# Optimization experiments

Hardware: AMD Instinct MI355X
Metric: run time of the kernel (lower is better)

The kernel has to match this reference:

```python
import jax, jax.numpy as jnp
import numpy as np

ORDER = 2


def _masked_row_mean(v, m, safe_cnt, has_any):
    # v already zeroed outside mask; per-row mean over masked entries
    s = jnp.sum(v, axis=1, keepdims=True) / safe_cnt
    return jnp.where(has_any, s, 0.0)


def high_order_residual(x, mask, order=ORDER):
    """Vectorized faithful version of high_order_residual (braq).
    nanmean over masked entries == masked sum / count; sign/scale/shift
    are only meaningful inside the mask, outputs outside the mask are 0.
    """
    m = mask.astype(x.dtype)                       # (oc, ic)
    cnt = jnp.sum(m, axis=1, keepdims=True)        # (oc, 1)
    safe_cnt = jnp.maximum(cnt, 1.0)
    has_any = cnt > 0
    xm = x * m
    sum_order = jnp.zeros_like(x)
    for _ in range(order):
        residual = (xm - sum_order) * m            # masked residual, 0 outside
        mean = _masked_row_mean(residual, m, safe_cnt, has_any)   # (oc,1)
        centered = (residual - mean) * m           # 0 outside mask
        scale = _masked_row_mean(jnp.abs(centered), m, safe_cnt, has_any)
        binary = jnp.sign(centered) * scale + mean
        sum_order = sum_order + binary * m
    return sum_order


def setup_inputs() -> dict:
    key = jax.random.key(0)
    k1, k2 = jax.random.split(key)
    x = jax.random.normal(k1, (11008, 4096), dtype=jnp.float32) * 0.02
    mask = jax.random.randint(k2, (11008, 4096), 0, 2).astype(jnp.bool_)
    return {"x": x, "mask": mask}


def reference(x, mask):
    return high_order_residual(x, mask, ORDER)
```

## Files before the change

kernel.cpp:

```cpp
#include <hip/hip_runtime.h>
#include <stdint.h>

#define IC      4096
#define BLK     256
#define RPB     4
#define CHUNKS  16
#define EPT     64

__global__ __launch_bounds__(BLK) void binarize_kernel(
    const float* __restrict__ x,
    const uint8_t* __restrict__ mask,
    float* __restrict__ out,
    int nrows)
{
    const int lane = threadIdx.x & 63;
    const int row  = blockIdx.x * RPB + (threadIdx.x >> 6);
    if (row >= nrows) return;

    const bool mask_is_i32 = !__any(((const uint32_t*)mask)[lane] > 1u);

    const float* xr   = x   + (size_t)row * IC;
    float*       orow = out + (size_t)row * IC;

    float xm[EPT];
    #pragma unroll
    for (int i = 0; i < CHUNKS; ++i) {
        float4 v = ((const float4*)xr)[lane + 64 * i];
        xm[4*i+0] = v.x; xm[4*i+1] = v.y; xm[4*i+2] = v.z; xm[4*i+3] = v.w;
    }

    uint32_t mw0 = 0, mw1 = 0;
    if (mask_is_i32) {
        const int4* mr = (const int4*)mask + (size_t)row * (IC / 4);
        #pragma unroll
        for (int i = 0; i < CHUNKS; ++i) {
            int4 m4 = mr[lane + 64 * i];
            uint32_t b = (uint32_t)(m4.x != 0)
                       | ((uint32_t)(m4.y != 0) << 1)
                       | ((uint32_t)(m4.z != 0) << 2)
                       | ((uint32_t)(m4.w != 0) << 3);
            if (i < 8) mw0 |= b << (4 * i);
            else       mw1 |= b << (4 * (i - 8));
        }
    } else {
        const uint32_t* mr = (const uint32_t*)(mask + (size_t)row * IC);
        #pragma unroll
        for (int i = 0; i < CHUNKS; ++i) {
            uint32_t w = mr[lane + 64 * i];
            uint32_t b = (uint32_t)((w & 0x000000ffu) != 0)
                       | ((uint32_t)((w & 0x0000ff00u) != 0) << 1)
                       | ((uint32_t)((w & 0x00ff0000u) != 0) << 2)
                       | ((uint32_t)((w & 0xff000000u) != 0) << 3);
            if (i < 8) mw0 |= b << (4 * i);
            else       mw1 |= b << (4 * (i - 8));
        }
    }

    #pragma unroll
    for (int j = 0; j < EPT; ++j) {
        const uint32_t bit = ((j < 32 ? mw0 : mw1) >> (j & 31)) & 1u;
        xm[j] = bit ? xm[j] : 0.f;
    }

    double sA0 = 0.0, sA1 = 0.0;
    #pragma unroll
    for (int j = 0; j < EPT; j += 2) {
        sA0 += (double)xm[j];
        sA1 += (double)xm[j + 1];
    }
    double s  = sA0 + sA1;
    float  cf = (float)(__popc(mw0) + __popc(mw1));
    #pragma unroll
    for (int off = 32; off; off >>= 1) {
        s  += __shfl_xor(s,  off);
        cf += __shfl_xor(cf, off);
    }

    const bool   has    = (cf > 0.f);
    const double c      = (double)cf;
    const double nmiss  = (double)(4096.f - cf);
    const double inv    = 1.0 / fmax(c, 1.0);
    const double mean1  = has ? s * inv : 0.0;
    const float  mean1f = (float)mean1;

    double saB0 = 0.0, saB1 = 0.0;
    float  dB0 = 0.f, dB1 = 0.f;
    #pragma unroll
    for (int j = 0; j < EPT; ++j) {
        const uint32_t bit = ((j < 32 ? mw0 : mw1) >> (j & 31)) & 1u;
        const float t   = xm[j] - mean1f;
        const float sg  = (t > 0.f) ? 1.f : ((t < 0.f) ? -1.f : 0.f);
        const float smv = bit ? sg : 0.f;
        if (j & 1) { dB1 += smv; saB1 += (double)fabsf(t); }
        else       { dB0 += smv; saB0 += (double)fabsf(t); }
    }
    double sa = saB0 + saB1;
    float  df = dB0 + dB1;
    #pragma unroll
    for (int off = 32; off; off >>= 1) {
        sa += __shfl_xor(sa, off);
        df += __shfl_xor(df, off);
    }
    sa -= nmiss * (double)fabsf(mean1f);

    const double scale1 = has ? sa * inv : 0.0;
    const double mean2  = has ? (s - scale1 * (double)df - mean1 * c) * inv : 0.0;
    const double mean12 = mean1 + mean2;

    double sb0 = 0.0, sb1 = 0.0;
    #pragma unroll
    for (int j = 0; j < EPT; ++j) {
        const uint32_t bit = ((j < 32 ? mw0 : mw1) >> (j & 31)) & 1u;
        const float t   = xm[j] - mean1f;
        const float sg  = (t > 0.f) ? 1.f : ((t < 0.f) ? -1.f : 0.f);
        const float smv = bit ? sg : 0.f;
        const double t2 = (double)xm[j] - fma((double)smv, scale1, mean12);
        if (j & 1) sb1 += fabs(t2); else sb0 += fabs(t2);
    }
    double sa2 = sb0 + sb1;
    #pragma unroll
    for (int off = 32; off; off >>= 1) sa2 += __shfl_xor(sa2, off);
    sa2 -= nmiss * fabs(mean12);
    const double scale2  = has ? sa2 * inv : 0.0;
    const float  scale2f = (float)scale2;

    #pragma unroll
    for (int i = 0; i < CHUNKS; ++i) {
        float r[4];
        #pragma unroll
        for (int k = 0; k < 4; ++k) {
            const int j = 4 * i + k;
            const uint32_t bit = ((j < 32 ? mw0 : mw1) >> (j & 31)) & 1u;
            const float t   = xm[j] - mean1f;
            const float sg  = (t > 0.f) ? 1.f : ((t < 0.f) ? -1.f : 0.f);
            const float smv = bit ? sg : 0.f;
            const double t2 = (double)xm[j] - fma((double)smv, scale1, mean12);
            const float t2f = (float)t2;
            const float b1f = xm[j] - t2f;
            const float sg2 = (t2f > 0.f) ? 1.f : ((t2f < 0.f) ? -1.f : 0.f);
            const float o   = fmaf(sg2, scale2f, b1f);
            r[k] = bit ? o : 0.f;
        }
        float4 o4; o4.x = r[0]; o4.y = r[1]; o4.z = r[2]; o4.w = r[3];
        ((float4*)orow)[lane + 64 * i] = o4;
    }
}

extern "C" void kernel_launch(void* const* d_in, const int* in_sizes, int n_in,
                              void* d_out, int out_size, void* d_ws, size_t ws_size,
                              hipStream_t stream) {
    const float*   x    = (const float*)d_in[0];
    const uint8_t* mask = (const uint8_t*)d_in[1];
    float*         out  = (float*)d_out;

    const int rows = in_sizes[0] / IC;
    const int grid = (rows + RPB - 1) / RPB;
    binarize_kernel<<<grid, BLK, 0, stream>>>(x, mask, out, rows);
}
```

Baseline: 418.1 us.

## Re-read row from global per pass instead of holding it in registers

The 64-element per-thread register array holding the masked row is removed. Each of the four passes now reloads the row from global memory (expected to hit in cache) and re-applies the mask bits. Launch bounds now request a minimum of 4 blocks per CU, which should allow more waves to be resident and better hide latency. The cost is three extra row reads per pass, served from L2 or the infinity cache, and a risk of becoming bandwidth-bound if those reads miss.

```diff
diff --git a/kernel.cpp b/kernel.cpp
--- a/kernel.cpp
+++ b/kernel.cpp
@@ -3,72 +3,60 @@
 
 #define IC      4096
 #define BLK     256
-#define RPB     4
+#define WPB     4
 #define CHUNKS  16
-#define EPT     64
 
-__global__ __launch_bounds__(BLK) void binarize_kernel(
+__global__ __launch_bounds__(BLK, 4) void binarize_kernel(
     const float* __restrict__ x,
     const uint8_t* __restrict__ mask,
     float* __restrict__ out,
     int nrows)
 {
     const int lane = threadIdx.x & 63;
-    const int row  = blockIdx.x * RPB + (threadIdx.x >> 6);
+    const int row  = blockIdx.x * WPB + (threadIdx.x >> 6);
     if (row >= nrows) return;
 
     const bool mask_is_i32 = !__any(((const uint32_t*)mask)[lane] > 1u);
 
-    const float* xr   = x   + (size_t)row * IC;
-    float*       orow = out + (size_t)row * IC;
-
-    float xm[EPT];
-    #pragma unroll
-    for (int i = 0; i < CHUNKS; ++i) {
-        float4 v = ((const float4*)xr)[lane + 64 * i];
-        xm[4*i+0] = v.x; xm[4*i+1] = v.y; xm[4*i+2] = v.z; xm[4*i+3] = v.w;
-    }
+    const float4* xr4 = (const float4*)(x + (size_t)row * IC);
+    float4*       or4 = (float4*)(out + (size_t)row * IC);
 
     uint32_t mw0 = 0, mw1 = 0;
+    double sacc[4] = {0.0, 0.0, 0.0, 0.0};
     if (mask_is_i32) {
         const int4* mr = (const int4*)mask + (size_t)row * (IC / 4);
         #pragma unroll
         for (int i = 0; i < CHUNKS; ++i) {
-            int4 m4 = mr[lane + 64 * i];
-            uint32_t b = (uint32_t)(m4.x != 0)
-                       | ((uint32_t)(m4.y != 0) << 1)
-                       | ((uint32_t)(m4.z != 0) << 2)
-                       | ((uint32_t)(m4.w != 0) << 3);
-            if (i < 8) mw0 |= b << (4 * i);
-            else       mw1 |= b << (4 * (i - 8));
+            const float4 v  = xr4[lane + 64 * i];
+            const int4   m4 = mr[lane + 64 * i];
+            const uint32_t b = (uint32_t)(m4.x != 0)
+                             | ((uint32_t)(m4.y != 0) << 1)
+                             | ((uint32_t)(m4.z != 0) << 2)
+                             | ((uint32_t)(m4.w != 0) << 3);
+            if (i < 8) mw0 |= b << (4 * i); else mw1 |= b << (4 * (i - 8));
+            sacc[0] += (double)((b & 1u) ? v.x : 0.f);
+            sacc[1] += (double)((b & 2u) ? v.y : 0.f);
+            sacc[2] += (double)((b & 4u) ? v.z : 0.f);
+            sacc[3] += (double)((b & 8u) ? v.w : 0.f);
         }
     } else {
         const uint32_t* mr = (const uint32_t*)(mask + (size_t)row * IC);
         #pragma unroll
         for (int i = 0; i < CHUNKS; ++i) {
-            uint32_t w = mr[lane + 64 * i];
-            uint32_t b = (uint32_t)((w & 0x000000ffu) != 0)
-                       | ((uint32_t)((w & 0x0000ff00u) != 0) << 1)
-                       | ((uint32_t)((w & 0x00ff0000u) != 0) << 2)
-                       | ((uint32_t)((w & 0xff000000u) != 0) << 3);
-            if (i < 8) mw0 |= b << (4 * i);
-            else       mw1 |= b << (4 * (i - 8));
+            const float4   v = xr4[lane + 64 * i];
+            const uint32_t w = mr[lane + 64 * i];
+            const uint32_t b = (uint32_t)((w & 0x000000ffu) != 0)
+                             | ((uint32_t)((w & 0x0000ff00u) != 0) << 1)
+                             | ((uint32_t)((w & 0x00ff0000u) != 0) << 2)
+                             | ((uint32_t)((w & 0xff000000u) != 0) << 3);
+            if (i < 8) mw0 |= b << (4 * i); else mw1 |= b << (4 * (i - 8));
+            sacc[0] += (double)((b & 1u) ? v.x : 0.f);
+            sacc[1] += (double)((b & 2u) ? v.y : 0.f);
+            sacc[2] += (double)((b & 4u) ? v.z : 0.f);
+            sacc[3] += (double)((b & 8u) ? v.w : 0.f);
         }
     }
-
-    #pragma unroll
-    for (int j = 0; j < EPT; ++j) {
-        const uint32_t bit = ((j < 32 ? mw0 : mw1) >> (j & 31)) & 1u;
-        xm[j] = bit ? xm[j] : 0.f;
-    }
-
-    double sA0 = 0.0, sA1 = 0.0;
-    #pragma unroll
-    for (int j = 0; j < EPT; j += 2) {
-        sA0 += (double)xm[j];
-        sA1 += (double)xm[j + 1];
-    }
-    double s  = sA0 + sA1;
+    double s  = (sacc[0] + sacc[1]) + (sacc[2] + sacc[3]);
     float  cf = (float)(__popc(mw0) + __popc(mw1));
     #pragma unroll
     for (int off = 32; off; off >>= 1) {
@@ -83,19 +71,24 @@
     const double mean1  = has ? s * inv : 0.0;
     const float  mean1f = (float)mean1;
 
-    double saB0 = 0.0, saB1 = 0.0;
-    float  dB0 = 0.f, dB1 = 0.f;
+    double saacc[4] = {0.0, 0.0, 0.0, 0.0};
+    float  dacc[4]  = {0.f, 0.f, 0.f, 0.f};
     #pragma unroll
-    for (int j = 0; j < EPT; ++j) {
-        const uint32_t bit = ((j < 32 ? mw0 : mw1) >> (j & 31)) & 1u;
-        const float t   = xm[j] - mean1f;
-        const float sg  = (t > 0.f) ? 1.f : ((t < 0.f) ? -1.f : 0.f);
-        const float smv = bit ? sg : 0.f;
-        if (j & 1) { dB1 += smv; saB1 += (double)fabsf(t); }
-        else       { dB0 += smv; saB0 += (double)fabsf(t); }
+    for (int i = 0; i < CHUNKS; ++i) {
+        const float4   v = xr4[lane + 64 * i];
+        const uint32_t b = ((i < 8) ? (mw0 >> (4 * i)) : (mw1 >> (4 * (i - 8)))) & 0xfu;
+        const float xe[4] = { (b & 1u) ? v.x : 0.f, (b & 2u) ? v.y : 0.f,
+                              (b & 4u) ? v.z : 0.f, (b & 8u) ? v.w : 0.f };
+        #pragma unroll
+        for (int k = 0; k < 4; ++k) {
+            const float t  = xe[k] - mean1f;
+            const float sg = (t > 0.f) ? 1.f : ((t < 0.f) ? -1.f : 0.f);
+            dacc[k]  += ((b >> k) & 1u) ? sg : 0.f;
+            saacc[k] += (double)fabsf(t);
+        }
     }
-    double sa = saB0 + saB1;
-    float  df = dB0 + dB1;
+    double sa = (saacc[0] + saacc[1]) + (saacc[2] + saacc[3]);
+    float  df = (dacc[0] + dacc[1]) + (dacc[2] + dacc[3]);
     #pragma unroll
     for (int off = 32; off; off >>= 1) {
         sa += __shfl_xor(sa, off);
@@ -107,17 +100,23 @@
     const double mean2  = has ? (s - scale1 * (double)df - mean1 * c) * inv : 0.0;
     const double mean12 = mean1 + mean2;
 
-    double sb0 = 0.0, sb1 = 0.0;
+    double sb[4] = {0.0, 0.0, 0.0, 0.0};
     #pragma unroll
-    for (int j = 0; j < EPT; ++j) {
-        const uint32_t bit = ((j < 32 ? mw0 : mw1) >> (j & 31)) & 1u;
-        const float t   = xm[j] - mean1f;
-        const float sg  = (t > 0.f) ? 1.f : ((t < 0.f) ? -1.f : 0.f);
-        const float smv = bit ? sg : 0.f;
-        const double t2 = (double)xm[j] - fma((double)smv, scale1, mean12);
-        if (j & 1) sb1 += fabs(t2); else sb0 += fabs(t2);
+    for (int i = 0; i < CHUNKS; ++i) {
+        const float4   v = xr4[lane + 64 * i];
+        const uint32_t b = ((i < 8) ? (mw0 >> (4 * i)) : (mw1 >> (4 * (i - 8)))) & 0xfu;
+        const float xe[4] = { (b & 1u) ? v.x : 0.f, (b & 2u) ? v.y : 0.f,
+                              (b & 4u) ? v.z : 0.f, (b & 8u) ? v.w : 0.f };
+        #pragma unroll
+        for (int k = 0; k < 4; ++k) {
+            const float t   = xe[k] - mean1f;
+            const float sg  = (t > 0.f) ? 1.f : ((t < 0.f) ? -1.f : 0.f);
+            const float smv = ((b >> k) & 1u) ? sg : 0.f;
+            const double t2 = (double)xe[k] - fma((double)smv, scale1, mean12);
+            sb[k] += fabs(t2);
+        }
     }
-    double sa2 = sb0 + sb1;
+    double sa2 = (sb[0] + sb[1]) + (sb[2] + sb[3]);
     #pragma unroll
     for (int off = 32; off; off >>= 1) sa2 += __shfl_xor(sa2, off);
     sa2 -= nmiss * fabs(mean12);
@@ -126,23 +125,25 @@
 
     #pragma unroll
     for (int i = 0; i < CHUNKS; ++i) {
+        const float4   v = xr4[lane + 64 * i];
+        const uint32_t b = ((i < 8) ? (mw0 >> (4 * i)) : (mw1 >> (4 * (i - 8)))) & 0xfu;
+        const float xe[4] = { (b & 1u) ? v.x : 0.f, (b & 2u) ? v.y : 0.f,
+                              (b & 4u) ? v.z : 0.f, (b & 8u) ? v.w : 0.f };
         float r[4];
         #pragma unroll
         for (int k = 0; k < 4; ++k) {
-            const int j = 4 * i + k;
-            const uint32_t bit = ((j < 32 ? mw0 : mw1) >> (j & 31)) & 1u;
-            const float t   = xm[j] - mean1f;
+            const float t   = xe[k] - mean1f;
             const float sg  = (t > 0.f) ? 1.f : ((t < 0.f) ? -1.f : 0.f);
-            const float smv = bit ? sg : 0.f;
-            const double t2 = (double)xm[j] - fma((double)smv, scale1, mean12);
+            const float smv = ((b >> k) & 1u) ? sg : 0.f;
+            const double t2 = (double)xe[k] - fma((double)smv, scale1, mean12);
             const float t2f = (float)t2;
-            const float b1f = xm[j] - t2f;
+            const float b1f = xe[k] - t2f;
             const float sg2 = (t2f > 0.f) ? 1.f : ((t2f < 0.f) ? -1.f : 0.f);
             const float o   = fmaf(sg2, scale2f, b1f);
-            r[k] = bit ? o : 0.f;
+            r[k] = ((b >> k) & 1u) ? o : 0.f;
         }
         float4 o4; o4.x = r[0]; o4.y = r[1]; o4.z = r[2]; o4.w = r[3];
-        ((float4*)orow)[lane + 64 * i] = o4;
+        or4[lane + 64 * i] = o4;
     }
 }
 
@@ -154,6 +155,6 @@
     float*         out  = (float*)d_out;
 
     const int rows = in_sizes[0] / IC;
-    const int grid = (rows + RPB - 1) / RPB;
+    const int grid = (rows + WPB - 1) / WPB;
     binarize_kernel<<<grid, BLK, 0, stream>>>(x, mask, out, rows);
 }
```

Measured after the change: 850.0 us. 103% more time.

## Process each row with a 512-thread block and prefetch the next row's data

Applied to the files above, without the earlier changes.

Switches from one wavefront per row (64 elements per thread) to a whole 512-thread block per row (8 elements per thread). Each block loops over 4 strided rows and prefetches the next row's x and mask into registers while the current row computes. Row reductions now go through shared memory with __syncthreads, and the first-pass sign values and second-pass residuals are cached in registers instead of being recomputed. The aim is to cut register pressure and raise occupancy and memory-level parallelism, at the cost of extra block-wide barriers per row.

```diff
diff --git a/kernel.cpp b/kernel.cpp
--- a/kernel.cpp
+++ b/kernel.cpp
@@ -1,80 +1,54 @@
 #include <hip/hip_runtime.h>
 #include <stdint.h>
 
-#define IC      4096
-#define BLK     256
-#define RPB     4
-#define CHUNKS  16
-#define EPT     64
+#define IC    4096
+#define BLK   512
+#define VPT   2
+#define EPT   8
+#define RPB   4
 
-__global__ __launch_bounds__(BLK) void binarize_kernel(
-    const float* __restrict__ x,
-    const uint8_t* __restrict__ mask,
-    float* __restrict__ out,
-    int nrows)
+__device__ __forceinline__ void bred_df(double& a, float& p, double* smd, float* smf) {
+    #pragma unroll
+    for (int off = 32; off; off >>= 1) { a += __shfl_xor(a, off); p += __shfl_xor(p, off); }
+    const int wid = threadIdx.x >> 6;
+    if ((threadIdx.x & 63) == 0) { smd[wid] = a; smf[wid] = p; }
+    __syncthreads();
+    a = ((smd[0]+smd[1])+(smd[2]+smd[3])) + ((smd[4]+smd[5])+(smd[6]+smd[7]));
+    p = ((smf[0]+smf[1])+(smf[2]+smf[3])) + ((smf[4]+smf[5])+(smf[6]+smf[7]));
+}
+
+__device__ __forceinline__ double bred_d(double a, double* smd) {
+    #pragma unroll
+    for (int off = 32; off; off >>= 1) a += __shfl_xor(a, off);
+    const int wid = threadIdx.x >> 6;
+    if ((threadIdx.x & 63) == 0) smd[wid] = a;
+    __syncthreads();
+    return ((smd[0]+smd[1])+(smd[2]+smd[3])) + ((smd[4]+smd[5])+(smd[6]+smd[7]));
+}
+
+__device__ __forceinline__ uint32_t byte4_to_bits(uint32_t w) {
+    return (uint32_t)((w & 0x000000ffu) != 0)
+         | ((uint32_t)((w & 0x0000ff00u) != 0) << 1)
+         | ((uint32_t)((w & 0x00ff0000u) != 0) << 2)
+         | ((uint32_t)((w & 0xff000000u) != 0) << 3);
+}
+
+__device__ __forceinline__ void row_compute(
+    const float (&xin)[EPT], uint32_t mb, float4* orow4,
+    int tid, double* smd, float* smf)
 {
-    const int lane = threadIdx.x & 63;
-    const int row  = blockIdx.x * RPB + (threadIdx.x >> 6);
-    if (row >= nrows) return;
-
-    const bool mask_is_i32 = !__any(((const uint32_t*)mask)[lane] > 1u);
-
-    const float* xr   = x   + (size_t)row * IC;
-    float*       orow = out + (size_t)row * IC;
-
     float xm[EPT];
-    #pragma unroll
-    for (int i = 0; i < CHUNKS; ++i) {
-        float4 v = ((const float4*)xr)[lane + 64 * i];
-        xm[4*i+0] = v.x; xm[4*i+1] = v.y; xm[4*i+2] = v.z; xm[4*i+3] = v.w;
-    }
-
-    uint32_t mw0 = 0, mw1 = 0;
-    if (mask_is_i32) {
-        const int4* mr = (const int4*)mask + (size_t)row * (IC / 4);
-        #pragma unroll
-        for (int i = 0; i < CHUNKS; ++i) {
-            int4 m4 = mr[lane + 64 * i];
-            uint32_t b = (uint32_t)(m4.x != 0)
-                       | ((uint32_t)(m4.y != 0) << 1)
-                       | ((uint32_t)(m4.z != 0) << 2)
-                       | ((uint32_t)(m4.w != 0) << 3);
-            if (i < 8) mw0 |= b << (4 * i);
-            else       mw1 |= b << (4 * (i - 8));
-        }
-    } else {
-        const uint32_t* mr = (const uint32_t*)(mask + (size_t)row * IC);
-        #pragma unroll
-        for (int i = 0; i < CHUNKS; ++i) {
-            uint32_t w = mr[lane + 64 * i];
-            uint32_t b = (uint32_t)((w & 0x000000ffu) != 0)
-                       | ((uint32_t)((w & 0x0000ff00u) != 0) << 1)
-                       | ((uint32_t)((w & 0x00ff0000u) != 0) << 2)
-                       | ((uint32_t)((w & 0xff000000u) != 0) << 3);
-            if (i < 8) mw0 |= b << (4 * i);
-            else       mw1 |= b << (4 * (i - 8));
-        }
-    }
+    float sgm[EPT];
 
     #pragma unroll
-    for (int j = 0; j < EPT; ++j) {
-        const uint32_t bit = ((j < 32 ? mw0 : mw1) >> (j & 31)) & 1u;
-        xm[j] = bit ? xm[j] : 0.f;
-    }
+    for (int j = 0; j < EPT; ++j) xm[j] = ((mb >> j) & 1u) ? xin[j] : 0.f;
 
-    double sA0 = 0.0, sA1 = 0.0;
+    double s0 = 0.0, s1 = 0.0;
     #pragma unroll
-    for (int j = 0; j < EPT; j += 2) {
-        sA0 += (double)xm[j];
-        sA1 += (double)xm[j + 1];
-    }
-    double s  = sA0 + sA1;
-    float  cf = (float)(__popc(mw0) + __popc(mw1));
-    #pragma unroll
-    for (int off = 32; off; off >>= 1) {
-        s  += __shfl_xor(s,  off);
-        cf += __shfl_xor(cf, off);
-    }
+    for (int j = 0; j < EPT; j += 2) { s0 += (double)xm[j]; s1 += (double)xm[j+1]; }
+    double s  = s0 + s1;
+    float  cf = (float)__popc(mb);
+    bred_df(s, cf, smd + 0, smf + 0);
 
     const bool   has    = (cf > 0.f);
     const double c      = (double)cf;
@@ -83,24 +57,20 @@
     const double mean1  = has ? s * inv : 0.0;
     const float  mean1f = (float)mean1;
 
-    double saB0 = 0.0, saB1 = 0.0;
-    float  dB0 = 0.f, dB1 = 0.f;
+    double sa0 = 0.0, sa1 = 0.0;
+    float  d0 = 0.f, d1 = 0.f;
     #pragma unroll
     for (int j = 0; j < EPT; ++j) {
-        const uint32_t bit = ((j < 32 ? mw0 : mw1) >> (j & 31)) & 1u;
-        const float t   = xm[j] - mean1f;
-        const float sg  = (t > 0.f) ? 1.f : ((t < 0.f) ? -1.f : 0.f);
-        const float smv = bit ? sg : 0.f;
-        if (j & 1) { dB1 += smv; saB1 += (double)fabsf(t); }
-        else       { dB0 += smv; saB0 += (double)fabsf(t); }
+        const float t  = xm[j] - mean1f;
+        const float sg = (t > 0.f) ? 1.f : ((t < 0.f) ? -1.f : 0.f);
+        const float sv = ((mb >> j) & 1u) ? sg : 0.f;
+        sgm[j] = sv;
+        if (j & 1) { d1 += sv; sa1 += (double)fabsf(t); }
+        else       { d0 += sv; sa0 += (double)fabsf(t); }
     }
-    double sa = saB0 + saB1;
-    float  df = dB0 + dB1;
-    #pragma unroll
-    for (int off = 32; off; off >>= 1) {
-        sa += __shfl_xor(sa, off);
-        df += __shfl_xor(df, off);
-    }
+    double sa = sa0 + sa1;
+    float  df = d0 + d1;
+    bred_df(sa, df, smd + 8, smf + 8);
     sa -= nmiss * (double)fabsf(mean1f);
 
     const double scale1 = has ? sa * inv : 0.0;
@@ -110,39 +80,90 @@
     double sb0 = 0.0, sb1 = 0.0;
     #pragma unroll
     for (int j = 0; j < EPT; ++j) {
-        const uint32_t bit = ((j < 32 ? mw0 : mw1) >> (j & 31)) & 1u;
-        const float t   = xm[j] - mean1f;
-        const float sg  = (t > 0.f) ? 1.f : ((t < 0.f) ? -1.f : 0.f);
-        const float smv = bit ? sg : 0.f;
-        const double t2 = (double)xm[j] - fma((double)smv, scale1, mean12);
+        const double t2 = (double)xm[j] - fma((double)sgm[j], scale1, mean12);
+        sgm[j] = (float)t2;
         if (j & 1) sb1 += fabs(t2); else sb0 += fabs(t2);
     }
-    double sa2 = sb0 + sb1;
-    #pragma unroll
-    for (int off = 32; off; off >>= 1) sa2 += __shfl_xor(sa2, off);
+    double sa2 = bred_d(sb0 + sb1, smd + 16);
     sa2 -= nmiss * fabs(mean12);
     const double scale2  = has ? sa2 * inv : 0.0;
     const float  scale2f = (float)scale2;
 
     #pragma unroll
-    for (int i = 0; i < CHUNKS; ++i) {
+    for (int i = 0; i < VPT; ++i) {
         float r[4];
         #pragma unroll
         for (int k = 0; k < 4; ++k) {
             const int j = 4 * i + k;
-            const uint32_t bit = ((j < 32 ? mw0 : mw1) >> (j & 31)) & 1u;
-            const float t   = xm[j] - mean1f;
-            const float sg  = (t > 0.f) ? 1.f : ((t < 0.f) ? -1.f : 0.f);
-            const float smv = bit ? sg : 0.f;
-            const double t2 = (double)xm[j] - fma((double)smv, scale1, mean12);
-            const float t2f = (float)t2;
+            const float t2f = sgm[j];
             const float b1f = xm[j] - t2f;
             const float sg2 = (t2f > 0.f) ? 1.f : ((t2f < 0.f) ? -1.f : 0.f);
-            const float o   = fmaf(sg2, scale2f, b1f);
-            r[k] = bit ? o : 0.f;
+            r[k] = ((mb >> j) & 1u) ? fmaf(sg2, scale2f, b1f) : 0.f;
         }
-        float4 o4; o4.x = r[0]; o4.y = r[1]; o4.z = r[2]; o4.w = r[3];
-        ((float4*)orow)[lane + 64 * i] = o4;
+        float4 o; o.x = r[0]; o.y = r[1]; o.z = r[2]; o.w = r[3];
+        orow4[tid + i * BLK] = o;
+    }
+}
+
+__global__ __launch_bounds__(BLK, 8) void binarize_kernel(
+    const float* __restrict__ x,
+    const uint8_t* __restrict__ mask,
+    float* __restrict__ out,
+    int nrows)
+{
+    __shared__ double smd[24];
+    __shared__ float  smf[16];
+    const int tid  = threadIdx.x;
+    const int lane = tid & 63;
+    const int S    = gridDim.x;
+
+    const bool mask_is_i32 = !__any(((const uint32_t*)mask)[lane] > 1u);
+
+    if (!mask_is_i32) {
+        float4   nxa, nxb;
+        uint32_t nma, nmb;
+        {
+            const int r = blockIdx.x;
+            const float4*   xr = (const float4*)(x + (size_t)r * IC);
+            const uint32_t* mr = (const uint32_t*)(mask + (size_t)r * IC);
+            nxa = xr[tid];       nxb = xr[tid + BLK];
+            nma = mr[tid];       nmb = mr[tid + BLK];
+        }
+        #pragma unroll
+        for (int k = 0; k < RPB; ++k) {
+            const int r = blockIdx.x + k * S;
+            if (r >= nrows) break;
+            float xin[EPT];
+            xin[0] = nxa.x; xin[1] = nxa.y; xin[2] = nxa.z; xin[3] = nxa.w;
+            xin[4] = nxb.x; xin[5] = nxb.y; xin[6] = nxb.z; xin[7] = nxb.w;
+            const uint32_t mb = byte4_to_bits(nma) | (byte4_to_bits(nmb) << 4);
+
+            const int rn = blockIdx.x + (k + 1) * S;
+            if (k + 1 < RPB && rn < nrows) {
+                const float4*   xr = (const float4*)(x + (size_t)rn * IC);
+                const uint32_t* mr = (const uint32_t*)(mask + (size_t)rn * IC);
+                nxa = xr[tid];   nxb = xr[tid + BLK];
+                nma = mr[tid];   nmb = mr[tid + BLK];
+            }
+            row_compute(xin, mb, (float4*)(out + (size_t)r * IC), tid, smd, smf);
+        }
+    } else {
+        for (int k = 0; k < RPB; ++k) {
+            const int r = blockIdx.x + k * S;
+            if (r >= nrows) break;
+            const float4* xr = (const float4*)(x + (size_t)r * IC);
+            const int4*   mr = (const int4*)mask + (size_t)r * (IC / 4);
+            float xin[EPT]; uint32_t mb = 0;
+            #pragma unroll
+            for (int i = 0; i < VPT; ++i) {
+                const float4 v  = xr[tid + i * BLK];
+                const int4   m4 = mr[tid + i * BLK];
+                xin[4*i+0] = v.x; xin[4*i+1] = v.y; xin[4*i+2] = v.z; xin[4*i+3] = v.w;
+                mb |= ((uint32_t)(m4.x != 0) | ((uint32_t)(m4.y != 0) << 1)
+                    |  ((uint32_t)(m4.z != 0) << 2) | ((uint32_t)(m4.w != 0) << 3)) << (4 * i);
+            }
+            row_compute(xin, mb, (float4*)(out + (size_t)r * IC), tid, smd, smf);
+        }
     }
 }
 
```

After: 417.9 us. Within noise of the previous version (-0.0%).
